# Optimization experiments

Hardware: AMD Instinct MI355X
Metric: run time of the kernel (lower is better)

The kernel has to match this reference:

```python
import jax, jax.numpy as jnp
import numpy as np

D_MODEL = 512
NHEAD = 8
HEAD_DIM = D_MODEL // NHEAD  # 64, also rotary_dim
WIN_LO, WIN_HI = 127, 128    # attn_window: kv in [q-127, q+128]
BLOCK = 256                  # block size for banded attention (>= WIN_LO+1 and >= WIN_HI)


def setup_inputs() -> dict:
    key = jax.random.key(0)
    k1, k2, k3, k4 = jax.random.split(key, 4)
    N, T = 4, 2048
    x = jax.random.normal(k1, (N, T, D_MODEL), dtype=jnp.float32)
    Wqkv_w = jax.random.normal(k2, (3 * D_MODEL, D_MODEL), dtype=jnp.float32) * 0.02
    out_w = jax.random.normal(k3, (D_MODEL, D_MODEL), dtype=jnp.float32) * 0.02
    out_b = jax.random.normal(k4, (D_MODEL,), dtype=jnp.float32) * 0.02
    return {"x": x, "Wqkv_w": Wqkv_w, "out_w": out_w, "out_b": out_b}


def _rotate_half(u):
    u1, u2 = jnp.split(u, 2, axis=-1)
    return jnp.concatenate((-u2, u1), axis=-1)


def _apply_rope(q, k, T, dtype):
    # inv_freq: [HEAD_DIM/2]
    inv_freq = 1.0 / (10000.0 ** (jnp.arange(0, HEAD_DIM, 2, dtype=jnp.float32) / HEAD_DIM))
    pos = jnp.arange(T, dtype=dtype)
    freqs = pos[:, None] * inv_freq[None, :].astype(dtype)      # [T, D/2]
    emb = jnp.concatenate((freqs, freqs), axis=-1)              # [T, D]
    cos = jnp.cos(emb)[None, :, None, :]                        # [1,T,1,D]
    sin = jnp.sin(emb)[None, :, None, :]
    q = q * cos + _rotate_half(q) * sin
    k = k * cos + _rotate_half(k) * sin
    return q, k


def reference(x, Wqkv_w, out_w, out_b):
    N, T, dm = x.shape
    H, D, B = NHEAD, HEAD_DIM, BLOCK
    qkv = (x @ Wqkv_w.T).reshape(N, T, 3, H, D)
    q, k, v = qkv[:, :, 0], qkv[:, :, 1], qkv[:, :, 2]          # [N,T,H,D]
    q, k = _apply_rope(q, k, T, x.dtype)
    # [N,H,T,D]
    q = q.transpose(0, 2, 1, 3)
    k = k.transpose(0, 2, 1, 3)
    v = v.transpose(0, 2, 1, 3)

    nb = T // B
    qb = q.reshape(N, H, nb, B, D)
    kb = k.reshape(N, H, nb, B, D)
    vb = v.reshape(N, H, nb, B, D)
    # pad one block of zeros on each side so block g sees key blocks g-1,g,g+1
    pad = ((0, 0), (0, 0), (1, 1), (0, 0), (0, 0))
    kp = jnp.pad(kb, pad)
    vp = jnp.pad(vb, pad)
    # [N,H,nb,3B,D]
    kwin = jnp.concatenate([kp[:, :, i:i + nb] for i in range(3)], axis=3)
    vwin = jnp.concatenate([vp[:, :, i:i + nb] for i in range(3)], axis=3)

    scale = 1.0 / np.sqrt(D)
    scores = jnp.einsum('nhgqd,nhgkd->nhgqk', qb, kwin) * scale  # [N,H,nb,B,3B]

    qi = jnp.arange(B)
    kj = jnp.arange(3 * B)
    gidx = jnp.arange(nb)
    diff = kj[None, None, :] - B - qi[None, :, None]             # [1,B,3B] kv - q offset
    band = (diff >= -WIN_LO) & (diff <= WIN_HI)
    kv_global = gidx[:, None, None] * B + kj[None, None, :] - B  # [nb,1,3B]
    valid = (kv_global >= 0) & (kv_global < T)
    mask = band & valid                                          # [nb,B,3B]

    neg = jnp.asarray(-1e30, dtype=scores.dtype)
    scores = jnp.where(mask[None, None], scores, neg)
    probs = jax.nn.softmax(scores, axis=-1)
    attn = jnp.einsum('nhgqk,nhgkd->nhgqd', probs, vwin)         # [N,H,nb,B,D]
    attn = attn.reshape(N, H, T, D).transpose(0, 2, 1, 3).reshape(N, T, dm)
    return attn @ out_w.T + out_b
```

## Files before the change

kernel.cpp:

```cpp
#include <hip/hip_runtime.h>
#include <math.h>


typedef __attribute__((ext_vector_type(8))) __bf16 bf16x8;
typedef __attribute__((ext_vector_type(4))) float f32x4;

__device__ __forceinline__ unsigned short f2bf(float f) {
    unsigned int u = __float_as_uint(f);
    u += 0x7fffu + ((u >> 16) & 1u);
    return (unsigned short)(u >> 16);
}
__device__ __forceinline__ unsigned int packbf2(float a, float b) {
    unsigned int ua = __float_as_uint(a); ua += 0x7fffu + ((ua >> 16) & 1u);
    unsigned int ub = __float_as_uint(b); ub += 0x7fffu + ((ub >> 16) & 1u);
    return (ua >> 16) | (ub & 0xffff0000u);
}
__device__ __forceinline__ bf16x8 as_bf16x8(uint4 u) {
    union { uint4 u4; bf16x8 v; } c; c.u4 = u; return c.v;
}
__device__ __forceinline__ bf16x8 ld_frag(const unsigned short* p) {
    return as_bf16x8(*(const uint4*)p);
}

__device__ __forceinline__ void async16(void* lds, const void* g) {
    __builtin_amdgcn_global_load_lds(
        (const __attribute__((address_space(1))) void*)g,
        (__attribute__((address_space(3))) void*)lds,
        16, 0, 0);
}

__global__ __launch_bounds__(256) void cvt_all(
    const float* __restrict__ x, const float* __restrict__ w1,
    const float* __restrict__ w2,
    unsigned short* __restrict__ xb, unsigned short* __restrict__ w1b,
    unsigned short* __restrict__ w2b)
{
    const int n_x  = 8192 * 512 / 4;
    const int n_w1 = 1536 * 512 / 4;
    const int n_w2 = 512 * 512 / 4;
    int i = blockIdx.x * 256 + threadIdx.x;
    const float* in; unsigned short* out; int j;
    if (i < n_x)                    { in = x;  out = xb;  j = i; }
    else if (i < n_x + n_w1)        { in = w1; out = w1b; j = i - n_x; }
    else if (i < n_x + n_w1 + n_w2) { in = w2; out = w2b; j = i - n_x - n_w1; }
    else return;
    float4 v = *(const float4*)(in + 4 * (size_t)j);
    uint2 o;
    o.x = packbf2(v.x, v.y);
    o.y = packbf2(v.z, v.w);
    *(uint2*)(out + 4 * (size_t)j) = o;
}

__global__ __launch_bounds__(256, 5) void gemm_bt_mfma(
    const unsigned short* __restrict__ A, const unsigned short* __restrict__ B,
    const float* __restrict__ bias, void* __restrict__ Cout,
    int M, int O, int K, int write_bf16, int do_rope,
    unsigned short* __restrict__ vT)
{
    __shared__ __align__(16) unsigned short As[128 * 64];
    __shared__ __align__(16) unsigned short Bs[64 * 64];

    const int tid  = threadIdx.x;
    const int wave = tid >> 6;
    const int lane = tid & 63;
    const int l15  = lane & 15;
    const int lg   = lane >> 4;
    const int row0 = blockIdx.x * 128;
    const int col0 = blockIdx.y * 64;
    const int wr   = wave * 32;

    f32x4 acc[2][4] = {};

    const int srow = tid >> 3;
    const int skg  = ((tid & 7) * 8) ^ ((srow & 7) * 8);
    const int fx   = (l15 & 7) * 8;

    for (int k0 = 0; k0 < K; k0 += 64) {
        #pragma unroll
        for (int s = 0; s < 4; ++s)
            async16(&As[(size_t)(s * 256 + tid) * 8],
                    A + (size_t)(row0 + s * 32 + srow) * K + k0 + skg);
        #pragma unroll
        for (int s = 0; s < 2; ++s)
            async16(&Bs[(size_t)(s * 256 + tid) * 8],
                    B + (size_t)(col0 + s * 32 + srow) * K + k0 + skg);
        __syncthreads();

        #pragma unroll
        for (int kstep = 0; kstep < 2; ++kstep) {
            const int kq = (kstep * 32 + lg * 8) ^ fx;
            bf16x8 af[2], bfr[4];
            #pragma unroll
            for (int mt = 0; mt < 2; ++mt)
                af[mt] = ld_frag(&As[(wr + mt * 16 + l15) * 64 + kq]);
            #pragma unroll
            for (int nt = 0; nt < 4; ++nt)
                bfr[nt] = ld_frag(&Bs[(nt * 16 + l15) * 64 + kq]);
            #pragma unroll
            for (int mt = 0; mt < 2; ++mt)
                #pragma unroll
                for (int nt = 0; nt < 4; ++nt)
                    acc[mt][nt] = __builtin_amdgcn_mfma_f32_16x16x32_bf16(
                        af[mt], bfr[nt], acc[mt][nt], 0, 0, 0);
        }
        __syncthreads();
    }

    const int qrow = lg * 4;

    if (do_rope && col0 < 1024) {
        const float cfreq = 0.28782313662425574f;
        const float invf0 = __expf(-(float)l15 * cfreq);
        const float invf1 = __expf(-(float)(16 + l15) * cfreq);
        #pragma unroll
        for (int mt = 0; mt < 2; ++mt) {
            #pragma unroll
            for (int r = 0; r < 4; ++r) {
                const int t = (row0 + wr + mt * 16 + qrow + r) & 2047;
                #pragma unroll
                for (int p = 0; p < 2; ++p) {
                    float ang = (float)t * (p ? invf1 : invf0);
                    float s, c;
                    __sincosf(ang, &s, &c);
                    float a = acc[mt][p][r];
                    float b = acc[mt][p + 2][r];
                    acc[mt][p][r]     = a * c - b * s;
                    acc[mt][p + 2][r] = b * c + a * s;
                }
            }
        }
        if (col0 < 512) {
            #pragma unroll
            for (int mt = 0; mt < 2; ++mt)
                #pragma unroll
                for (int nt = 0; nt < 4; ++nt)
                    #pragma unroll
                    for (int r = 0; r < 4; ++r)
                        acc[mt][nt][r] *= 0.125f;
        }
    }

    if (do_rope && col0 >= 1024) {
        #pragma unroll
        for (int nt = 0; nt < 4; ++nt) {
            const int local = col0 - 1024 + nt * 16 + l15;
            const int hh = local >> 6;
            const int dd = local & 63;
            #pragma unroll
            for (int mt = 0; mt < 2; ++mt) {
                const int rowb = row0 + wr + mt * 16 + qrow;
                const int nn = rowb >> 11;
                const int tt = rowb & 2047;
                uint2 o;
                o.x = packbf2(acc[mt][nt][0], acc[mt][nt][1]);
                o.y = packbf2(acc[mt][nt][2], acc[mt][nt][3]);
                *(uint2*)(vT + ((size_t)(nn * 8 + hh) * 64 + dd) * 2048 + tt) = o;
            }
        }
        return;
    }

    #pragma unroll
    for (int nt = 0; nt < 4; ++nt) {
        const int col = col0 + nt * 16 + l15;
        const float bv = bias ? bias[col] : 0.f;
        #pragma unroll
        for (int mt = 0; mt < 2; ++mt) {
            const int rowb = row0 + wr + mt * 16 + qrow;
            if (write_bf16) {
                unsigned short* C = (unsigned short*)Cout;
                #pragma unroll
                for (int r = 0; r < 4; ++r)
                    C[(size_t)(rowb + r) * O + col] = f2bf(acc[mt][nt][r] + bv);
            } else {
                float* C = (float*)Cout;
                #pragma unroll
                for (int r = 0; r < 4; ++r)
                    C[(size_t)(rowb + r) * O + col] = acc[mt][nt][r] + bv;
            }
        }
    }
}

__global__ __launch_bounds__(256) void attn_mfma_kernel(
    const unsigned short* __restrict__ qkv,
    const unsigned short* __restrict__ vT,
    unsigned short* __restrict__ attnout)
{
    __shared__ __align__(16) unsigned short Kt[64 * 72];
    __shared__ __align__(16) unsigned short Vt[64 * 72];
    __shared__ __align__(16) unsigned short Ps[4][16 * 72];

    const int qt = blockIdx.x;
    const int h  = blockIdx.y;
    const int n  = blockIdx.z;
    const int t0 = qt * 64;
    const int tid  = threadIdx.x;
    const int wave = tid >> 6;
    const int lane = tid & 63;
    const int l15  = lane & 15;
    const int lg   = lane >> 4;

    const size_t base = (size_t)n * 2048 * 1536 + (size_t)h * 64;
    const unsigned short* vTh = vT + (size_t)(n * 8 + h) * 64 * 2048;

    bf16x8 qfrag[2];
    {
        const unsigned short* qp = qkv + base + (size_t)(t0 + wave * 16 + l15) * 1536;
        qfrag[0] = ld_frag(qp + lg * 8);
        qfrag[1] = ld_frag(qp + 32 + lg * 8);
    }

    const int skey = tid >> 2;
    const int sd0  = (tid & 3) * 16;

    float m_r[4], l_r[4];
    #pragma unroll
    for (int r = 0; r < 4; ++r) { m_r[r] = -1e30f; l_r[r] = 0.f; }
    f32x4 acc_o[4] = {};

    for (int dt = -2; dt <= 2; ++dt) {
        const int kt = qt + dt;
        if (kt < 0 || kt > 31) continue;
        const int s0 = kt * 64;

        {
            const unsigned short* kp = qkv + base + 512 + (size_t)(s0 + skey) * 1536 + sd0;
            *(uint4*)&Kt[skey * 72 + sd0]     = *(const uint4*)kp;
            *(uint4*)&Kt[skey * 72 + sd0 + 8] = *(const uint4*)(kp + 8);

            const unsigned short* vp = vTh + (size_t)skey * 2048 + s0 + sd0;
            *(uint4*)&Vt[skey * 72 + sd0]     = *(const uint4*)vp;
            *(uint4*)&Vt[skey * 72 + sd0 + 8] = *(const uint4*)(vp + 8);
        }
        __syncthreads();

        f32x4 acc_s[4] = {};
        #pragma unroll
        for (int kstep = 0; kstep < 2; ++kstep) {
            #pragma unroll
            for (int nt = 0; nt < 4; ++nt) {
                if ((dt == -2 && nt < wave) || (dt == 2 && nt > wave)) continue;
                bf16x8 kf = ld_frag(&Kt[(nt * 16 + l15) * 72 + kstep * 32 + lg * 8]);
                acc_s[nt] = __builtin_amdgcn_mfma_f32_16x16x32_bf16(
                    qfrag[kstep], kf, acc_s[nt], 0, 0, 0);
            }
        }

        float sc[4][4];
        #pragma unroll
        for (int nt = 0; nt < 4; ++nt) {
            const int key_off = dt * 64 + nt * 16 + l15;
            #pragma unroll
            for (int r = 0; r < 4; ++r) {
                const int diff = key_off - (wave * 16 + lg * 4 + r);
                const bool ok = (diff >= -127) && (diff <= 128);
                sc[nt][r] = ok ? acc_s[nt][r] : -1e30f;
            }
        }
        #pragma unroll
        for (int r = 0; r < 4; ++r) {
            float tm = fmaxf(fmaxf(sc[0][r], sc[1][r]), fmaxf(sc[2][r], sc[3][r]));
            tm = fmaxf(tm, __shfl_xor(tm, 1, 64));
            tm = fmaxf(tm, __shfl_xor(tm, 2, 64));
            tm = fmaxf(tm, __shfl_xor(tm, 4, 64));
            tm = fmaxf(tm, __shfl_xor(tm, 8, 64));
            const float m_new = fmaxf(m_r[r], tm);
            const float alpha = __expf(m_r[r] - m_new);
            float psum = 0.f;
            #pragma unroll
            for (int nt = 0; nt < 4; ++nt) {
                float p = __expf(sc[nt][r] - m_new);
                sc[nt][r] = p;
                psum += p;
            }
            psum += __shfl_xor(psum, 1, 64);
            psum += __shfl_xor(psum, 2, 64);
            psum += __shfl_xor(psum, 4, 64);
            psum += __shfl_xor(psum, 8, 64);
            l_r[r] = l_r[r] * alpha + psum;
            m_r[r] = m_new;
            #pragma unroll
            for (int nt = 0; nt < 4; ++nt) acc_o[nt][r] *= alpha;
        }

        #pragma unroll
        for (int nt = 0; nt < 4; ++nt)
            #pragma unroll
            for (int r = 0; r < 4; ++r)
                Ps[wave][(lg * 4 + r) * 72 + nt * 16 + l15] = f2bf(sc[nt][r]);

        __syncthreads();

        bf16x8 pfrag[2];
        pfrag[0] = ld_frag(&Ps[wave][l15 * 72 + lg * 8]);
        pfrag[1] = ld_frag(&Ps[wave][l15 * 72 + 32 + lg * 8]);

        #pragma unroll
        for (int kstep = 0; kstep < 2; ++kstep) {
            #pragma unroll
            for (int nt = 0; nt < 4; ++nt) {
                bf16x8 vf = ld_frag(&Vt[(nt * 16 + l15) * 72 + kstep * 32 + lg * 8]);
                acc_o[nt] = __builtin_amdgcn_mfma_f32_16x16x32_bf16(
                    pfrag[kstep], vf, acc_o[nt], 0, 0, 0);
            }
        }
        __syncthreads();
    }

    float inv_l[4];
    #pragma unroll
    for (int r = 0; r < 4; ++r) inv_l[r] = 1.0f / l_r[r];

    #pragma unroll
    for (int r = 0; r < 4; ++r) {
        const int tq = t0 + wave * 16 + lg * 4 + r;
        unsigned short* op = attnout + (size_t)(n * 2048 + tq) * 512 + h * 64;
        #pragma unroll
        for (int nt = 0; nt < 4; ++nt)
            op[nt * 16 + l15] = f2bf(acc_o[nt][r] * inv_l[r]);
    }
}

extern "C" void kernel_launch(void* const* d_in, const int* in_sizes, int n_in,
                              void* d_out, int out_size, void* d_ws, size_t ws_size,
                              hipStream_t stream)
{
    (void)in_sizes; (void)n_in; (void)out_size; (void)ws_size;

    const float* x     = (const float*)d_in[0];
    const float* Wqkv  = (const float*)d_in[1];
    const float* out_w = (const float*)d_in[2];
    const float* out_b = (const float*)d_in[3];
    float* out = (float*)d_out;

    unsigned short* qkvb  = (unsigned short*)d_ws;
    unsigned short* attnb = qkvb + (size_t)8192 * 1536;
    unsigned short* xb    = attnb + (size_t)8192 * 512;
    unsigned short* wqkvb = xb + (size_t)8192 * 512;
    unsigned short* outwb = wqkvb + (size_t)1536 * 512;
    unsigned short* vTb   = outwb + (size_t)512 * 512;

    cvt_all<<<5120, 256, 0, stream>>>(x, Wqkv, out_w, xb, wqkvb, outwb);

    gemm_bt_mfma<<<dim3(64, 24), 256, 0, stream>>>(xb, wqkvb, nullptr, qkvb,
                                                   8192, 1536, 512, 1, 1, vTb);
    attn_mfma_kernel<<<dim3(32, 8, 4), 256, 0, stream>>>(qkvb, vTb, attnb);
    gemm_bt_mfma<<<dim3(64, 8), 256, 0, stream>>>(attnb, outwb, out_b, out,
                                                  8192, 512, 512, 0, 0, nullptr);
}
```

Before: 130.3 us.

## Prefetch next K/V tile into registers and drop per-wave P barrier

Loads the next key/value tile from global memory into registers while the current tile's QK^T, softmax and PV run, then stores it to LDS at the start of the next iteration. This hides global load latency behind the compute. It also removes the block-wide barrier between writing the per-wave probability tile and reading it back, since each wave uses its own Ps slice. The cost is extra registers per thread and reliance on intra-wave LDS ordering.

```diff
diff --git a/kernel.cpp b/kernel.cpp
--- a/kernel.cpp
+++ b/kernel.cpp
@@ -219,21 +219,36 @@
     for (int r = 0; r < 4; ++r) { m_r[r] = -1e30f; l_r[r] = 0.f; }
     f32x4 acc_o[4] = {};
 
-    for (int dt = -2; dt <= 2; ++dt) {
-        const int kt = qt + dt;
-        if (kt < 0 || kt > 31) continue;
-        const int s0 = kt * 64;
-
-        {
-            const unsigned short* kp = qkv + base + 512 + (size_t)(s0 + skey) * 1536 + sd0;
-            *(uint4*)&Kt[skey * 72 + sd0]     = *(const uint4*)kp;
-            *(uint4*)&Kt[skey * 72 + sd0 + 8] = *(const uint4*)(kp + 8);
-
-            const unsigned short* vp = vTh + (size_t)skey * 2048 + s0 + sd0;
-            *(uint4*)&Vt[skey * 72 + sd0]     = *(const uint4*)vp;
-            *(uint4*)&Vt[skey * 72 + sd0 + 8] = *(const uint4*)(vp + 8);
-        }
+    const int dt_lo = (qt >= 2) ? -2 : -qt;
+    const int dt_hi = (qt <= 29) ? 2 : 31 - qt;
+
+    uint4 rk0, rk1, rv0, rv1;
+    {
+        const int s0 = (qt + dt_lo) * 64;
+        const unsigned short* kp = qkv + base + 512 + (size_t)(s0 + skey) * 1536 + sd0;
+        rk0 = *(const uint4*)kp;
+        rk1 = *(const uint4*)(kp + 8);
+        const unsigned short* vp = vTh + (size_t)skey * 2048 + s0 + sd0;
+        rv0 = *(const uint4*)vp;
+        rv1 = *(const uint4*)(vp + 8);
+    }
+
+    for (int dt = dt_lo; dt <= dt_hi; ++dt) {
+        *(uint4*)&Kt[skey * 72 + sd0]     = rk0;
+        *(uint4*)&Kt[skey * 72 + sd0 + 8] = rk1;
+        *(uint4*)&Vt[skey * 72 + sd0]     = rv0;
+        *(uint4*)&Vt[skey * 72 + sd0 + 8] = rv1;
         __syncthreads();
+
+        if (dt < dt_hi) {
+            const int s1 = (qt + dt + 1) * 64;
+            const unsigned short* kp = qkv + base + 512 + (size_t)(s1 + skey) * 1536 + sd0;
+            rk0 = *(const uint4*)kp;
+            rk1 = *(const uint4*)(kp + 8);
+            const unsigned short* vp = vTh + (size_t)skey * 2048 + s1 + sd0;
+            rv0 = *(const uint4*)vp;
+            rv1 = *(const uint4*)(vp + 8);
+        }
 
         f32x4 acc_s[4] = {};
         #pragma unroll
@@ -290,8 +305,6 @@
             for (int r = 0; r < 4; ++r)
                 Ps[wave][(lg * 4 + r) * 72 + nt * 16 + l15] = f2bf(sc[nt][r]);
 
-        __syncthreads();
-
         bf16x8 pfrag[2];
         pfrag[0] = ld_frag(&Ps[wave][l15 * 72 + lg * 8]);
         pfrag[1] = ld_frag(&Ps[wave][l15 * 72 + 32 + lg * 8]);
```

New measurement: 135.4 us. 1.04x slower.
